# Performance work log

Measured on AMD Instinct MI355X. Metric: run time of the kernel, lower is better.

## Reference

```python
import jax, jax.numpy as jnp
import numpy as np

C_CONST = 0.0  # polynomial kernel additive constant (init arg c)
D_CONST = 2    # polynomial kernel degree (init arg d)


def setup_inputs() -> dict:
    key = jax.random.key(0)
    k1, k2 = jax.random.split(key)
    input = jax.random.normal(k1, (1, 64, 128, 64), dtype=jnp.float32)
    target = jax.random.normal(k2, (1, 64, 128, 64), dtype=jnp.float32)
    return {"input": input, "target": target}


def reference(input, target):
    ch = input.shape[1]
    hw_input = input.shape[2] * input.shape[3]
    hw_target = target.shape[2] * target.shape[3]
    # Flatten to [hw, c] feature matrices (batch assumed 1, as in the original view(c, -1).T)
    F = input.reshape(ch, -1).T   # [hw_input, c]
    S = target.reshape(ch, -1).T  # [hw_target, c]

    def kernel(A, B):
        # Naive polynomial kernel Gram matrix: (A @ B^T + c)^d
        return (A @ B.T + C_CONST) ** D_CONST

    loss = kernel(F, F) + kernel(S, S) - 2.0 * kernel(F, S)
    return loss.sum() / hw_input / hw_target / (ch ** 2)
```

## Files before the change

### kernel.cpp

```cpp
#include <hip/hip_runtime.h>


#define CH    64
#define KTOT  8192
#define G1    256
#define KPB   (KTOT / G1)
#define CHUNK 16
#define NCHUNK (KPB / CHUNK)

#define NORMF 3.637978807091713e-12f

__global__ __launch_bounds__(256) void gram_partial(
    const float* __restrict__ in, const float* __restrict__ tg,
    float* __restrict__ ws)
{
    __shared__ __attribute__((aligned(16))) float ts_in[CHUNK][CH];
    __shared__ __attribute__((aligned(16))) float ts_tg[CHUNK][CH];

    const int t   = threadIdx.x;
    const int blk = blockIdx.x;
    const int k0  = blk * KPB;

    const int lch = t >> 2;
    const int lko = (t & 3) << 2;

    const int ty = t >> 4;
    const int tx = t & 15;
    const int a0 = ty << 2;
    const int b0 = tx << 2;

    float acc[4][4];
#pragma unroll
    for (int i = 0; i < 4; ++i)
#pragma unroll
        for (int j = 0; j < 4; ++j) acc[i][j] = 0.f;

#pragma unroll
    for (int c = 0; c < NCHUNK; ++c) {
        const int kc = k0 + c * CHUNK;
        const float4 vi = *(const float4*)(in + lch * KTOT + kc + lko);
        const float4 vt = *(const float4*)(tg + lch * KTOT + kc + lko);
        ts_in[lko + 0][lch] = vi.x; ts_in[lko + 1][lch] = vi.y;
        ts_in[lko + 2][lch] = vi.z; ts_in[lko + 3][lch] = vi.w;
        ts_tg[lko + 0][lch] = vt.x; ts_tg[lko + 1][lch] = vt.y;
        ts_tg[lko + 2][lch] = vt.z; ts_tg[lko + 3][lch] = vt.w;
        __syncthreads();

#pragma unroll
        for (int kk = 0; kk < CHUNK; ++kk) {
            const float4 av = *(const float4*)&ts_in[kk][a0];
            const float4 bv = *(const float4*)&ts_in[kk][b0];
            const float4 cv = *(const float4*)&ts_tg[kk][a0];
            const float4 dv = *(const float4*)&ts_tg[kk][b0];
            const float aa[4] = {av.x, av.y, av.z, av.w};
            const float bb[4] = {bv.x, bv.y, bv.z, bv.w};
            const float cc[4] = {cv.x, cv.y, cv.z, cv.w};
            const float dd[4] = {dv.x, dv.y, dv.z, dv.w};
#pragma unroll
            for (int i = 0; i < 4; ++i)
#pragma unroll
                for (int j = 0; j < 4; ++j) {
                    acc[i][j] = fmaf(aa[i], bb[j], acc[i][j]);
                    acc[i][j] = fmaf(-cc[i], dd[j], acc[i][j]);
                }
        }
        __syncthreads();
    }

    float* p = ws + blk * 4096;
#pragma unroll
    for (int i = 0; i < 4; ++i) {
        float4 v;
        v.x = acc[i][0]; v.y = acc[i][1]; v.z = acc[i][2]; v.w = acc[i][3];
        *(float4*)(p + (a0 + i) * 64 + b0) = v;
    }
}

__global__ __launch_bounds__(256) void reduce_square(
    const float* __restrict__ ws, float* __restrict__ out)
{
    __shared__ float red[4][64];
    const int t  = threadIdx.x;
    const int el = t & 63;
    const int e  = (blockIdx.x << 6) + el;
    const int sl = t >> 6;

    float s = 0.f;
    const int p0 = sl * (G1 / 4);
#pragma unroll 8
    for (int p = p0; p < p0 + (G1 / 4); ++p)
        s += ws[p * 4096 + e];
    red[sl][el] = s;
    __syncthreads();

    if (sl == 0) {
        float tot = red[0][el] + red[1][el] + red[2][el] + red[3][el];
        float sq  = tot * tot;
#pragma unroll
        for (int off = 32; off > 0; off >>= 1)
            sq += __shfl_down(sq, off);
        if (el == 0) atomicAdd(out, sq * NORMF);
    }
}

extern "C" void kernel_launch(void* const* d_in, const int* in_sizes, int n_in,
                              void* d_out, int out_size, void* d_ws, size_t ws_size,
                              hipStream_t stream)
{
    const float* in = (const float*)d_in[0];
    const float* tg = (const float*)d_in[1];
    float* out = (float*)d_out;
    float* ws  = (float*)d_ws;

    hipMemsetAsync(out, 0, sizeof(float), stream);
    gram_partial<<<G1, 256, 0, stream>>>(in, tg, ws);
    reduce_square<<<64, 256, 0, stream>>>(ws, out);
}
```

Measured before the change: 65.93 us.

## Split K across more blocks and intra-block groups with smem reduction

```diff
diff --git a/kernel.cpp b/kernel.cpp
--- a/kernel.cpp
+++ b/kernel.cpp
@@ -3,31 +3,40 @@
 
 #define CH    64
 #define KTOT  8192
-#define G1    256
+#define G1    512
 #define KPB   (KTOT / G1)
-#define CHUNK 16
-#define NCHUNK (KPB / CHUNK)
+#define NGRP  2
+#define KPG   (KPB / NGRP)
 
 #define NORMF 3.637978807091713e-12f
 
-__global__ __launch_bounds__(256) void gram_partial(
+__global__ __launch_bounds__(512, 4) void gram_partial(
     const float* __restrict__ in, const float* __restrict__ tg,
     float* __restrict__ ws)
 {
-    __shared__ __attribute__((aligned(16))) float ts_in[CHUNK][CH];
-    __shared__ __attribute__((aligned(16))) float ts_tg[CHUNK][CH];
+    __shared__ __attribute__((aligned(16))) float ts_in[KPB][CH];
+    __shared__ __attribute__((aligned(16))) float ts_tg[KPB][CH];
+    __shared__ __attribute__((aligned(16))) float red[4096];
 
-    const int t   = threadIdx.x;
-    const int blk = blockIdx.x;
-    const int k0  = blk * KPB;
+    const int t  = threadIdx.x;
+    const int k0 = blockIdx.x * KPB;
 
-    const int lch = t >> 2;
-    const int lko = (t & 3) << 2;
+    {
+        const int lch = t >> 3;
+        const int lko = (t & 7) << 1;
+        const float2 vi = *(const float2*)(in + lch * KTOT + k0 + lko);
+        const float2 vt = *(const float2*)(tg + lch * KTOT + k0 + lko);
+        ts_in[lko + 0][lch] = vi.x; ts_in[lko + 1][lch] = vi.y;
+        ts_tg[lko + 0][lch] = vt.x; ts_tg[lko + 1][lch] = vt.y;
+    }
+    __syncthreads();
 
-    const int ty = t >> 4;
-    const int tx = t & 15;
-    const int a0 = ty << 2;
-    const int b0 = tx << 2;
+    const int g   = t >> 8;
+    const int tid = t & 255;
+    const int ty  = tid >> 4;
+    const int tx  = tid & 15;
+    const int a0  = ty << 2;
+    const int b0  = tx << 2;
 
     float acc[4][4];
 #pragma unroll
@@ -36,70 +45,72 @@
         for (int j = 0; j < 4; ++j) acc[i][j] = 0.f;
 
 #pragma unroll
-    for (int c = 0; c < NCHUNK; ++c) {
-        const int kc = k0 + c * CHUNK;
-        const float4 vi = *(const float4*)(in + lch * KTOT + kc + lko);
-        const float4 vt = *(const float4*)(tg + lch * KTOT + kc + lko);
-        ts_in[lko + 0][lch] = vi.x; ts_in[lko + 1][lch] = vi.y;
-        ts_in[lko + 2][lch] = vi.z; ts_in[lko + 3][lch] = vi.w;
-        ts_tg[lko + 0][lch] = vt.x; ts_tg[lko + 1][lch] = vt.y;
-        ts_tg[lko + 2][lch] = vt.z; ts_tg[lko + 3][lch] = vt.w;
-        __syncthreads();
-
+    for (int kk = g * KPG; kk < g * KPG + KPG; ++kk) {
+        const float4 av = *(const float4*)&ts_in[kk][a0];
+        const float4 bv = *(const float4*)&ts_in[kk][b0];
+        const float4 cv = *(const float4*)&ts_tg[kk][a0];
+        const float4 dv = *(const float4*)&ts_tg[kk][b0];
+        const float aa[4] = {av.x, av.y, av.z, av.w};
+        const float bb[4] = {bv.x, bv.y, bv.z, bv.w};
+        const float cc[4] = {cv.x, cv.y, cv.z, cv.w};
+        const float dd[4] = {dv.x, dv.y, dv.z, dv.w};
 #pragma unroll
-        for (int kk = 0; kk < CHUNK; ++kk) {
-            const float4 av = *(const float4*)&ts_in[kk][a0];
-            const float4 bv = *(const float4*)&ts_in[kk][b0];
-            const float4 cv = *(const float4*)&ts_tg[kk][a0];
-            const float4 dv = *(const float4*)&ts_tg[kk][b0];
-            const float aa[4] = {av.x, av.y, av.z, av.w};
-            const float bb[4] = {bv.x, bv.y, bv.z, bv.w};
-            const float cc[4] = {cv.x, cv.y, cv.z, cv.w};
-            const float dd[4] = {dv.x, dv.y, dv.z, dv.w};
+        for (int i = 0; i < 4; ++i)
 #pragma unroll
-            for (int i = 0; i < 4; ++i)
-#pragma unroll
-                for (int j = 0; j < 4; ++j) {
-                    acc[i][j] = fmaf(aa[i], bb[j], acc[i][j]);
-                    acc[i][j] = fmaf(-cc[i], dd[j], acc[i][j]);
-                }
-        }
-        __syncthreads();
+            for (int j = 0; j < 4; ++j) {
+                acc[i][j] = fmaf(aa[i], bb[j], acc[i][j]);
+                acc[i][j] = fmaf(-cc[i], dd[j], acc[i][j]);
+            }
     }
 
-    float* p = ws + blk * 4096;
+    if (g == 1) {
 #pragma unroll
-    for (int i = 0; i < 4; ++i) {
-        float4 v;
-        v.x = acc[i][0]; v.y = acc[i][1]; v.z = acc[i][2]; v.w = acc[i][3];
-        *(float4*)(p + (a0 + i) * 64 + b0) = v;
+        for (int i = 0; i < 4; ++i) {
+            float4 v;
+            v.x = acc[i][0]; v.y = acc[i][1]; v.z = acc[i][2]; v.w = acc[i][3];
+            *(float4*)&red[tid * 16 + i * 4] = v;
+        }
+    }
+    __syncthreads();
+    if (g == 0) {
+        float* p = ws + blockIdx.x * 4096;
+#pragma unroll
+        for (int i = 0; i < 4; ++i) {
+            const float4 r = *(const float4*)&red[tid * 16 + i * 4];
+            float4 v;
+            v.x = acc[i][0] + r.x; v.y = acc[i][1] + r.y;
+            v.z = acc[i][2] + r.z; v.w = acc[i][3] + r.w;
+            *(float4*)(p + (a0 + i) * 64 + b0) = v;
+        }
     }
 }
 
 __global__ __launch_bounds__(256) void reduce_square(
     const float* __restrict__ ws, float* __restrict__ out)
 {
-    __shared__ float red[4][64];
+    __shared__ float red2[8][32];
     const int t  = threadIdx.x;
-    const int el = t & 63;
-    const int e  = (blockIdx.x << 6) + el;
-    const int sl = t >> 6;
+    const int el = t & 31;
+    const int sl = t >> 5;
+    const int e  = (blockIdx.x << 5) + el;
 
     float s = 0.f;
-    const int p0 = sl * (G1 / 4);
-#pragma unroll 8
-    for (int p = p0; p < p0 + (G1 / 4); ++p)
+    const int p0 = sl * (G1 / 8);
+#pragma unroll 16
+    for (int p = p0; p < p0 + (G1 / 8); ++p)
         s += ws[p * 4096 + e];
-    red[sl][el] = s;
+    red2[sl][el] = s;
     __syncthreads();
 
-    if (sl == 0) {
-        float tot = red[0][el] + red[1][el] + red[2][el] + red[3][el];
-        float sq  = tot * tot;
+    if (t < 32) {
+        float tot = 0.f;
 #pragma unroll
-        for (int off = 32; off > 0; off >>= 1)
+        for (int i = 0; i < 8; ++i) tot += red2[i][t];
+        float sq = tot * tot;
+#pragma unroll
+        for (int off = 16; off > 0; off >>= 1)
             sq += __shfl_down(sq, off);
-        if (el == 0) atomicAdd(out, sq * NORMF);
+        if (t == 0) atomicAdd(out, sq * NORMF);
     }
 }
 
@@ -113,6 +124,6 @@
     float* ws  = (float*)d_ws;
 
     hipMemsetAsync(out, 0, sizeof(float), stream);
-    gram_partial<<<G1, 256, 0, stream>>>(in, tg, ws);
-    reduce_square<<<64, 256, 0, stream>>>(ws, out);
+    gram_partial<<<G1, 512, 0, stream>>>(in, tg, ws);
+    reduce_square<<<128, 256, 0, stream>>>(ws, out);
 }
```

Result: slower. 67.30 us (+2.1%).
